# Kernel tuning notes

Hardware: AMD Instinct MI355X
Metric: run time of the kernel (lower is better)

Reference implementation:

```python
import jax, jax.numpy as jnp
import numpy as np

N_QUBITS = 20
N_PART = 10  # log2(out_features=1024)
W_MUL = (2.0 ** 0.5) * (5.0 ** -0.5)  # he_std * lrmul with gain=sqrt(2), lrmul=1

_H = (jnp.array([[1.0, 1.0], [1.0, -1.0]], dtype=jnp.complex64) / jnp.sqrt(jnp.array(2.0, jnp.float32)))


def _rx(theta):
    c = jnp.cos(theta * 0.5).astype(jnp.complex64)
    s = (-1j * jnp.sin(theta * 0.5)).astype(jnp.complex64)
    return jnp.stack([jnp.stack([c, s]), jnp.stack([s, c])])


def _ry(theta):
    c = jnp.cos(theta * 0.5).astype(jnp.complex64)
    s = jnp.sin(theta * 0.5).astype(jnp.complex64)
    return jnp.stack([jnp.stack([c, -s]), jnp.stack([s, c])])


def _rz(theta):
    e = jnp.exp(-0.5j * theta.astype(jnp.complex64))
    z = jnp.zeros((), jnp.complex64)
    return jnp.stack([jnp.stack([e, z]), jnp.stack([z, jnp.conj(e)])])


def _apply_1q(state, gate, q):
    # Apply 2x2 gate on qubit q (qubit 0 = most significant bit, matching kron order).
    s = state.reshape(2 ** q, 2, -1)
    return jnp.einsum('ab,ibj->iaj', gate, s).reshape(-1)


def _apply_cnot(state, c, t, n):
    a, b = (c, t) if c < t else (t, c)
    s = state.reshape(2 ** a, 2, 2 ** (b - a - 1), 2, 2 ** (n - b - 1))
    if c < t:
        # control at axis 1; after slicing, target is axis 2
        s = s.at[:, 1].set(jnp.flip(s[:, 1], axis=2))
    else:
        # control at axis 3; after slicing, target is axis 1
        s = s.at[:, :, :, 1].set(jnp.flip(s[:, :, :, 1], axis=1))
    return s.reshape(-1)


def setup_inputs() -> dict:
    key = jax.random.key(0)
    kx, kw = jax.random.split(key)
    x = jax.random.normal(kx, (1, N_QUBITS), dtype=jnp.float32)
    weight = jax.random.uniform(kw, (3 * N_QUBITS,), dtype=jnp.float32,
                                minval=0.0, maxval=2.0 * np.pi)
    return {"x": x, "weight": weight}


def reference(x, weight):
    n = N_QUBITS
    xq = jnp.squeeze(x)  # (n_qubits,)
    state = jnp.zeros(2 ** n, dtype=jnp.complex64).at[0].set(1.0 + 0j)
    # encoding layer: H, ry(arctan(x)), rz(arctan(x^2)) on each qubit
    for q in range(n):
        state = _apply_1q(state, _H, q)
        state = _apply_1q(state, _ry(jnp.arctan(xq[q])), q)
        state = _apply_1q(state, _rz(jnp.arctan(xq[q] * xq[q])), q)
    # variational layer: ring of CNOTs (q -> q+1, q -> q+2), then rx,rz,rx
    w = weight * W_MUL
    for q in range(n):
        state = _apply_cnot(state, q, (q + 1) % n, n)
        state = _apply_cnot(state, q, (q + 2) % n, n)
    for q in range(n):
        state = _apply_1q(state, _rx(w[3 * q + 0]), q)
        state = _apply_1q(state, _rz(w[3 * q + 1]), q)
        state = _apply_1q(state, _rx(w[3 * q + 2]), q)
    # partial measurement of the first N_PART (most significant) qubits:
    # marginalize |amp|^2 over the remaining qubits
    probs = (jnp.abs(state) ** 2).astype(jnp.float32)
    hidden = probs.reshape(2 ** N_PART, -1).sum(axis=1)
    return hidden[None, :]  # (1, 2**N_PART)
```

## Files before the change

### kernel.cpp

```cpp
#include <hip/hip_runtime.h>
#include <cstdint>


#define NQ     20
#define NPART  10
#define NH     1024
#define NL     1024
#define BLOCK  256
#define NBLOCKS 256
#define LPB    (NL / NBLOCKS)

struct MaskArg { uint32_t m[NQ]; };

__device__ __forceinline__ float2 cmul(float2 a, float2 b) {
    return make_float2(fmaf(a.x, b.x, -a.y * b.y), fmaf(a.x, b.y, a.y * b.x));
}
__device__ __forceinline__ float2 cadd(float2 a, float2 b) {
    return make_float2(a.x + b.x, a.y + b.y);
}

__global__ __launch_bounds__(BLOCK) void qulinear_kernel(
        const float* __restrict__ x, const float* __restrict__ w,
        float* __restrict__ out, MaskArg masks) {
    __shared__ float2 v[NQ][2];
    __shared__ float2 U[NPART][2][2];
    __shared__ float2 psi[NH];
    __shared__ float  hid[NH];

    const int tid = threadIdx.x;

    if (tid < NQ) {
        float xq = x[tid];
        float th = atanf(xq);
        float ph = atanf(xq * xq);
        float c, s, cp, sp;
        __sincosf(0.5f * th, &s, &c);
        __sincosf(0.5f * ph, &sp, &cp);
        float a = (c - s) * 0.70710678118654752f;
        float b = (c + s) * 0.70710678118654752f;
        v[tid][0] = make_float2(a * cp, -a * sp);
        v[tid][1] = make_float2(b * cp,  b * sp);
    }
    if (tid < NPART) {
        const float WM = 0.63245553203367590f;
        float a0 = w[3 * tid + 0] * WM;
        float a1 = w[3 * tid + 1] * WM;
        float a2 = w[3 * tid + 2] * WM;
        float c0, s0, c1, s1, c2, s2;
        __sincosf(0.5f * a0, &s0, &c0);
        __sincosf(0.5f * a1, &s1, &c1);
        __sincosf(0.5f * a2, &s2, &c2);
        float2 e0 = make_float2(c1, -s1), e1 = make_float2(c1, s1);
        float2 m00 = cmul(e0, make_float2(c0, 0.f));
        float2 m01 = cmul(e0, make_float2(0.f, -s0));
        float2 m10 = cmul(e1, make_float2(0.f, -s0));
        float2 m11 = cmul(e1, make_float2(c0, 0.f));
        float2 r00 = make_float2(c2, 0.f), r01 = make_float2(0.f, -s2);
        U[tid][0][0] = cadd(cmul(r00, m00), cmul(r01, m10));
        U[tid][0][1] = cadd(cmul(r00, m01), cmul(r01, m11));
        U[tid][1][0] = cadd(cmul(r01, m00), cmul(r00, m10));
        U[tid][1][1] = cadd(cmul(r01, m01), cmul(r00, m11));
    }
    #pragma unroll
    for (int k = 0; k < NH / BLOCK; ++k) hid[tid + k * BLOCK] = 0.f;
    __syncthreads();

    for (int il = 0; il < LPB; ++il) {
        const uint32_t l = (uint32_t)(blockIdx.x * LPB + il);

        #pragma unroll
        for (int k = 0; k < NH / BLOCK; ++k) {
            int h = tid + k * BLOCK;
            uint32_t y = ((uint32_t)h << NPART) | l;
            float2 amp = make_float2(1.f, 0.f);
            #pragma unroll
            for (int q = 0; q < NQ; ++q) {
                int bit = __popc(masks.m[q] & y) & 1;
                amp = cmul(amp, v[q][bit]);
            }
            psi[h] = amp;
        }
        __syncthreads();

        #pragma unroll
        for (int q = 0; q < NPART; ++q) {
            const int p = (NPART - 1) - q;
            #pragma unroll
            for (int j = tid; j < NH / 2; j += BLOCK) {
                int lo = j & ((1 << p) - 1);
                int h0 = ((j >> p) << (p + 1)) | lo;
                int h1 = h0 | (1 << p);
                float2 a = psi[h0], b = psi[h1];
                float2 na = cadd(cmul(U[q][0][0], a), cmul(U[q][0][1], b));
                float2 nb = cadd(cmul(U[q][1][0], a), cmul(U[q][1][1], b));
                psi[h0] = na;
                psi[h1] = nb;
            }
            __syncthreads();
        }

        #pragma unroll
        for (int k = 0; k < NH / BLOCK; ++k) {
            int h = tid + k * BLOCK;
            float2 a = psi[h];
            hid[h] += fmaf(a.x, a.x, a.y * a.y);
        }
        __syncthreads();
    }

    #pragma unroll
    for (int k = 0; k < NH / BLOCK; ++k) {
        int i = tid + k * BLOCK;
        atomicAdd(&out[i], hid[i]);
    }
}

extern "C" void kernel_launch(void* const* d_in, const int* in_sizes, int n_in,
                              void* d_out, int out_size, void* d_ws, size_t ws_size,
                              hipStream_t stream) {
    const float* x = (const float*)d_in[0];
    const float* w = (const float*)d_in[1];
    float* out = (float*)d_out;

    MaskArg ma;
    {
        uint32_t M[NQ];
        for (int q = 0; q < NQ; ++q) M[q] = 1u << q;
        for (int q = NQ - 1; q >= 0; --q) {
            M[(q + 2) % NQ] ^= M[q];
            M[(q + 1) % NQ] ^= M[q];
        }
        for (int q = 0; q < NQ; ++q) {
            uint32_t im = 0;
            for (int j = 0; j < NQ; ++j)
                if ((M[q] >> j) & 1) im |= 1u << (NQ - 1 - j);
            ma.m[q] = im;
        }
    }

    hipMemsetAsync(d_out, 0, (size_t)out_size * sizeof(float), stream);
    qulinear_kernel<<<NBLOCKS, BLOCK, 0, stream>>>(x, w, out, ma);
}
```

Measured before the change: 80.66 us.

## Map each wave to one low index, keep amplitudes in registers with shuffle butterflies

Each wavefront now handles one low-qubit index l, and each lane holds 16 amplitudes in registers. The parity bits come from a small shared table combined by XOR, so the per-amplitude popcount loop is no longer needed. The 10 one-qubit gates are applied with cross-lane shuffles for the low 6 bits and in-register butterflies for the high 4 bits. This replaces the shared-memory psi array and its ten __syncthreads per l, in exchange for more register pressure and shuffle traffic.

```diff
diff --git a/kernel.cpp b/kernel.cpp
--- a/kernel.cpp
+++ b/kernel.cpp
@@ -2,13 +2,11 @@
 #include <cstdint>
 
 
-#define NQ     20
-#define NPART  10
-#define NH     1024
-#define NL     1024
-#define BLOCK  256
+#define NQ      20
+#define NPART   10
+#define NH      1024
+#define BLOCK   256
 #define NBLOCKS 256
-#define LPB    (NL / NBLOCKS)
 
 struct MaskArg { uint32_t m[NQ]; };
 
@@ -22,10 +20,10 @@
 __global__ __launch_bounds__(BLOCK) void qulinear_kernel(
         const float* __restrict__ x, const float* __restrict__ w,
         float* __restrict__ out, MaskArg masks) {
-    __shared__ float2 v[NQ][2];
-    __shared__ float2 U[NPART][2][2];
-    __shared__ float2 psi[NH];
-    __shared__ float  hid[NH];
+    __shared__ float2   v[NQ][2];
+    __shared__ float2   U[NPART][2][2];
+    __shared__ uint32_t stab[16];
+    __shared__ float    hid[4][NH];
 
     const int tid = threadIdx.x;
 
@@ -61,57 +59,90 @@
         U[tid][1][0] = cadd(cmul(r01, m00), cmul(r00, m10));
         U[tid][1][1] = cadd(cmul(r01, m01), cmul(r00, m11));
     }
-    #pragma unroll
-    for (int k = 0; k < NH / BLOCK; ++k) hid[tid + k * BLOCK] = 0.f;
+    if (tid < 16) {
+        uint32_t y = (uint32_t)tid << 16;
+        uint32_t s = 0;
+        #pragma unroll
+        for (int q = 0; q < NQ; ++q)
+            s |= (uint32_t)(__popc(masks.m[q] & y) & 1) << q;
+        stab[tid] = s;
+    }
     __syncthreads();
 
-    for (int il = 0; il < LPB; ++il) {
-        const uint32_t l = (uint32_t)(blockIdx.x * LPB + il);
+    const int wave = tid >> 6;
+    const int lane = tid & 63;
+    const uint32_t l = (uint32_t)(blockIdx.x * 4 + wave);
 
+    const uint32_t y0 = ((uint32_t)lane << NPART) | l;
+    uint32_t sbase = 0;
+    #pragma unroll
+    for (int q = 0; q < NQ; ++q)
+        sbase |= (uint32_t)(__popc(masks.m[q] & y0) & 1) << q;
+
+    uint32_t s[16];
+    #pragma unroll
+    for (int r = 0; r < 16; ++r) s[r] = sbase ^ stab[r];
+
+    float2 amp[16];
+    #pragma unroll
+    for (int r = 0; r < 16; ++r) amp[r] = make_float2(1.f, 0.f);
+
+    #pragma unroll 4
+    for (int q = 0; q < NQ; ++q) {
+        float2 v0 = v[q][0], v1 = v[q][1];
         #pragma unroll
-        for (int k = 0; k < NH / BLOCK; ++k) {
-            int h = tid + k * BLOCK;
-            uint32_t y = ((uint32_t)h << NPART) | l;
-            float2 amp = make_float2(1.f, 0.f);
-            #pragma unroll
-            for (int q = 0; q < NQ; ++q) {
-                int bit = __popc(masks.m[q] & y) & 1;
-                amp = cmul(amp, v[q][bit]);
-            }
-            psi[h] = amp;
+        for (int r = 0; r < 16; ++r) {
+            bool b = (s[r] >> q) & 1u;
+            float2 sel = make_float2(b ? v1.x : v0.x, b ? v1.y : v0.y);
+            amp[r] = cmul(amp[r], sel);
         }
-        __syncthreads();
-
-        #pragma unroll
-        for (int q = 0; q < NPART; ++q) {
-            const int p = (NPART - 1) - q;
-            #pragma unroll
-            for (int j = tid; j < NH / 2; j += BLOCK) {
-                int lo = j & ((1 << p) - 1);
-                int h0 = ((j >> p) << (p + 1)) | lo;
-                int h1 = h0 | (1 << p);
-                float2 a = psi[h0], b = psi[h1];
-                float2 na = cadd(cmul(U[q][0][0], a), cmul(U[q][0][1], b));
-                float2 nb = cadd(cmul(U[q][1][0], a), cmul(U[q][1][1], b));
-                psi[h0] = na;
-                psi[h1] = nb;
-            }
-            __syncthreads();
-        }
-
-        #pragma unroll
-        for (int k = 0; k < NH / BLOCK; ++k) {
-            int h = tid + k * BLOCK;
-            float2 a = psi[h];
-            hid[h] += fmaf(a.x, a.x, a.y * a.y);
-        }
-        __syncthreads();
     }
 
     #pragma unroll
+    for (int p = 0; p < 6; ++p) {
+        const int lm = 1 << p;
+        const bool bit = (lane & lm) != 0;
+        float2 g00 = U[9 - p][0][0], g01 = U[9 - p][0][1];
+        float2 g10 = U[9 - p][1][0], g11 = U[9 - p][1][1];
+        float2 ga = bit ? g11 : g00;
+        float2 gb = bit ? g10 : g01;
+        #pragma unroll
+        for (int r = 0; r < 16; ++r) {
+            float2 mine = amp[r];
+            float2 oth = make_float2(__shfl_xor(mine.x, lm, 64),
+                                     __shfl_xor(mine.y, lm, 64));
+            amp[r] = cadd(cmul(ga, mine), cmul(gb, oth));
+        }
+    }
+
+    #pragma unroll
+    for (int p = 6; p < 10; ++p) {
+        const int pb = p - 6;
+        float2 g00 = U[9 - p][0][0], g01 = U[9 - p][0][1];
+        float2 g10 = U[9 - p][1][0], g11 = U[9 - p][1][1];
+        #pragma unroll
+        for (int j = 0; j < 8; ++j) {
+            int lo = j & ((1 << pb) - 1);
+            int r0 = ((j >> pb) << (pb + 1)) | lo;
+            int r1 = r0 | (1 << pb);
+            float2 a = amp[r0], b = amp[r1];
+            amp[r0] = cadd(cmul(g00, a), cmul(g01, b));
+            amp[r1] = cadd(cmul(g10, a), cmul(g11, b));
+        }
+    }
+
+    #pragma unroll
+    for (int r = 0; r < 16; ++r) {
+        int h = (r << 6) | lane;
+        hid[wave][h] = fmaf(amp[r].x, amp[r].x, amp[r].y * amp[r].y);
+    }
+    __syncthreads();
+
+    #pragma unroll
     for (int k = 0; k < NH / BLOCK; ++k) {
-        int i = tid + k * BLOCK;
-        atomicAdd(&out[i], hid[i]);
+        int h = tid + k * BLOCK;
+        float acc = hid[0][h] + hid[1][h] + hid[2][h] + hid[3][h];
+        atomicAdd(&out[h], acc);
     }
 }
 
```

Result: faster. 74.04 us (-8.2%).
